# Kernel tuning notes

Hardware: AMD Instinct MI355X
Metric: run time of the kernel (lower is better)

Reference implementation:

```python
import jax, jax.numpy as jnp
import numpy as np

N_NODES = 100000
N_EDGES = 400000
N_GRAPHS = 5000
F_IN = 64
H = 128
OUT = 1
N_LAYERS = 3  # gat_conv + 2 atom_gats
NEG_SLOPE = 0.01


def _gat_conv(x_src, x_dst, src, dst, W, a_src, a_dst, b, num_dst):
    """PyG GATConv, heads=1, add_self_loops=False, negative_slope=0.01.

    x_src: [Ns, Fin], x_dst: [Nd, Fin]; src/dst: [E] int; W: [Fin, H];
    a_src, a_dst, b: [H]. Returns [Nd, H].
    """
    hs = x_src @ W                      # [Ns, H]
    hd = x_dst @ W                      # [Nd, H]
    as_n = hs @ a_src                   # [Ns]
    ad_n = hd @ a_dst                   # [Nd]
    e = jax.nn.leaky_relu(as_n[src] + ad_n[dst], NEG_SLOPE)  # [E]
    # segment softmax over destination nodes
    seg_max = jax.ops.segment_max(e, dst, num_segments=num_dst)
    seg_max = jnp.where(jnp.isfinite(seg_max), seg_max, 0.0)
    ex = jnp.exp(e - seg_max[dst])
    denom = jax.ops.segment_sum(ex, dst, num_segments=num_dst) + 1e-16
    alpha = ex / denom[dst]             # [E]
    out = jax.ops.segment_sum(alpha[:, None] * hs[src], dst, num_segments=num_dst)
    return out + b


def setup_inputs() -> dict:
    key = jax.random.key(0)
    ks = jax.random.split(key, 16)
    x = jax.random.normal(ks[0], (N_NODES, F_IN), dtype=jnp.float32)
    edge_index = jax.random.randint(ks[1], (2, N_EDGES), 0, N_NODES, dtype=jnp.int64)
    batch = jnp.sort(jax.random.randint(ks[2], (N_NODES,), 0, N_GRAPHS, dtype=jnp.int64))
    s_in = 1.0 / np.sqrt(F_IN)
    s_h = 1.0 / np.sqrt(H)
    W1 = jax.random.uniform(ks[3], (F_IN, H), jnp.float32, -s_in, s_in)
    b1 = jax.random.uniform(ks[4], (H,), jnp.float32, -s_in, s_in)
    gW = jax.random.normal(ks[5], (N_LAYERS, H, H), jnp.float32) * s_h
    g_asrc = jax.random.normal(ks[6], (N_LAYERS, H), jnp.float32) * s_h
    g_adst = jax.random.normal(ks[7], (N_LAYERS, H), jnp.float32) * s_h
    g_b = jnp.zeros((N_LAYERS, H), jnp.float32)
    mW = jax.random.normal(ks[8], (H, H), jnp.float32) * s_h
    m_asrc = jax.random.normal(ks[9], (H,), jnp.float32) * s_h
    m_adst = jax.random.normal(ks[10], (H,), jnp.float32) * s_h
    m_b = jnp.zeros((H,), jnp.float32)
    W2 = jax.random.uniform(ks[11], (H, OUT), jnp.float32, -s_h, s_h)
    b2 = jax.random.uniform(ks[12], (OUT,), jnp.float32, -s_h, s_h)
    return {"x": x, "edge_index": edge_index, "batch": batch,
            "W1": W1, "b1": b1, "gW": gW, "g_asrc": g_asrc,
            "g_adst": g_adst, "g_b": g_b, "mW": mW, "m_asrc": m_asrc,
            "m_adst": m_adst, "m_b": m_b, "W2": W2, "b2": b2}


def reference(x, edge_index, batch, W1, b1, gW, g_asrc, g_adst, g_b,
              mW, m_asrc, m_adst, m_b, W2, b2):
    src, dst = edge_index[0], edge_index[1]
    h = jax.nn.leaky_relu(x @ W1 + b1, NEG_SLOPE)            # lin1 + leaky_relu_
    for i in range(N_LAYERS):                                 # gat_conv + atom_gats
        h = jax.nn.elu(_gat_conv(h, h, src, dst, gW[i], g_asrc[i],
                                 g_adst[i], g_b[i], N_NODES))
    # global readout: node -> graph bipartite GAT
    pooled = jax.nn.relu(jax.ops.segment_sum(h, batch, num_segments=N_GRAPHS))
    row = jnp.arange(N_NODES)
    out = jax.nn.elu(_gat_conv(h, pooled, row, batch, mW, m_asrc,
                               m_adst, m_b, N_GRAPHS))
    return out @ W2 + b2                                      # [N_GRAPHS, OUT]
```

## Files before the change

kernel.cpp:

```cpp
#include <hip/hip_runtime.h>
#include <hip/hip_fp16.h>
#include <math.h>
#include <stdint.h>

#define DEV __device__ __forceinline__

using f32x4 = __attribute__((ext_vector_type(4))) float;
using half8 = __attribute__((ext_vector_type(8))) _Float16;
typedef union { uint4 u; half8 h; } u4h8;

DEV float lrelu(float x){ return x > 0.f ? x : 0.01f*x; }
DEV float elu1(float x){ return x > 0.f ? x : __expf(x)-1.f; }

DEV int lower_bound_i(const int* __restrict__ a, int n, int key){
  int lo = 0, hi = n;
  while (lo < hi){ int mid = (lo+hi)>>1; if (a[mid] < key) lo = mid+1; else hi = mid; }
  return lo;
}

__global__ void xprep(const float* __restrict__ x, unsigned short* __restrict__ xh, int n4){
  int i = blockIdx.x*256 + threadIdx.x;
  if (i >= n4) return;
  float4 v = ((const float4*)x)[i];
  __half2 h0 = __floats2half2_rn(v.x, v.y);
  __half2 h1 = __floats2half2_rn(v.z, v.w);
  uint2 o;
  o.x = *(uint32_t*)&h0; o.y = *(uint32_t*)&h1;
  *(uint2*)(xh + (size_t)i*4) = o;
}

__global__ void wprep(const float* __restrict__ W, unsigned short* __restrict__ Hi,
                      unsigned short* __restrict__ Lo, int K, int tot){
  int idx = blockIdx.x*256 + threadIdx.x;
  if (idx >= tot) return;
  int kn = K*128;
  int mat = idx / kn;
  int rem = idx - mat*kn;
  int k = rem >> 7;
  int n = rem & 127;
  float v = W[idx];
  __half h = __float2half_rn(v);
  float lo = (v - __half2float(h)) * 1024.f;
  size_t o = (size_t)mat*kn + (size_t)n*K + k;
  Hi[o] = __half_as_ushort(h);
  Lo[o] = __half_as_ushort(__float2half_rn(lo));
}

template<int KC, int OUTMODE, bool DOTA, bool DOTB>
__global__ __launch_bounds__(256, 3) void gemm_mfma(
    const unsigned short* __restrict__ Ah, const unsigned short* __restrict__ Wt_hi,
    const unsigned short* __restrict__ Wt_lo, const float* __restrict__ bias,
    const float* __restrict__ va, const float* __restrict__ vb,
    unsigned short* __restrict__ Ch,
    float* __restrict__ outa, float* __restrict__ outb, int M)
{
  constexpr int K = KC*32;
  const int tid = threadIdx.x;
  const int lane = tid & 63;
  const int wv = tid >> 6;
  const int ml = lane & 15;
  const int kg = lane >> 4;
  const int R0 = blockIdx.x * 64;

  __shared__ uint32_t sA[2][1024];
  __shared__ float sC[4][32][36];
  __shared__ float sd[4][64][2];

  const unsigned short* bhp[2];
  const unsigned short* blp[2];
  #pragma unroll
  for (int nt = 0; nt < 2; ++nt){
    int n = wv*32 + nt*16 + ml;
    bhp[nt] = Wt_hi + (size_t)n*K + kg*8;
    blp[nt] = Wt_lo + (size_t)n*K + kg*8;
  }

  auto STAGE = [&](int c){
    int o = tid*16;
    int row = o >> 6;
    int t = (o >> 4) & 3;
    int gr = R0 + row; gr = gr < M ? gr : M-1;
    int j = t ^ ((row >> 1) & 3);
    const char* src = (const char*)(Ah + (size_t)gr*K + c*32) + j*16;
    char* dst = (char*)(&sA[c & 1][0]) + wv*1024;
    __builtin_amdgcn_global_load_lds(
        (const __attribute__((address_space(1))) void*)src,
        (__attribute__((address_space(3))) void*)dst, 16, 0, 0);
  };

  f32x4 accH[4][2], accL[4][2];
  #pragma unroll
  for (int mt = 0; mt < 4; ++mt)
    #pragma unroll
    for (int nt = 0; nt < 2; ++nt){
      accH[mt][nt] = (f32x4){0.f,0.f,0.f,0.f};
      accL[mt][nt] = (f32x4){0.f,0.f,0.f,0.f};
    }

  STAGE(0);
  u4h8 bhC[2], blC[2];
  #pragma unroll
  for (int nt = 0; nt < 2; ++nt){
    bhC[nt].u = *(const uint4*)(bhp[nt]);
    blC[nt].u = *(const uint4*)(blp[nt]);
  }
  __syncthreads();

  #pragma unroll
  for (int c = 0; c < KC; ++c){
    u4h8 bhN[2], blN[2];
    if (c + 1 < KC){
      STAGE(c + 1);
      #pragma unroll
      for (int nt = 0; nt < 2; ++nt){
        bhN[nt].u = *(const uint4*)(bhp[nt] + (c+1)*32);
        blN[nt].u = *(const uint4*)(blp[nt] + (c+1)*32);
      }
    }
    const char* buf = (const char*)&sA[c & 1][0];
    #pragma unroll
    for (int mt = 0; mt < 4; ++mt){
      int row = mt*16 + ml;
      int ba = row*64 + ((kg ^ ((row >> 1) & 3)) * 16);
      u4h8 A_;
      A_.u = *(const uint4*)(buf + ba);
      #pragma unroll
      for (int nt = 0; nt < 2; ++nt){
        accH[mt][nt] = __builtin_amdgcn_mfma_f32_16x16x32_f16(A_.h, bhC[nt].h, accH[mt][nt], 0, 0, 0);
        accL[mt][nt] = __builtin_amdgcn_mfma_f32_16x16x32_f16(A_.h, blC[nt].h, accL[mt][nt], 0, 0, 0);
      }
    }
    __syncthreads();
    if (c + 1 < KC){
      #pragma unroll
      for (int nt = 0; nt < 2; ++nt){ bhC[nt] = bhN[nt]; blC[nt] = blN[nt]; }
    }
  }

  #pragma unroll
  for (int mt = 0; mt < 4; ++mt)
    #pragma unroll
    for (int nt = 0; nt < 2; ++nt)
      accH[mt][nt] = accH[mt][nt] + accL[mt][nt] * 9.765625e-4f;

  if constexpr (DOTA || DOTB){
    float vaL[2] = {0.f,0.f}, vbL[2] = {0.f,0.f};
    if constexpr (DOTA){ vaL[0] = va[wv*32 + ml]; vaL[1] = va[wv*32 + 16 + ml]; }
    if constexpr (DOTB){ vbL[0] = vb[wv*32 + ml]; vbL[1] = vb[wv*32 + 16 + ml]; }
    #pragma unroll
    for (int mt = 0; mt < 4; ++mt){
      #pragma unroll
      for (int r = 0; r < 4; ++r){
        float pa = 0.f, pb = 0.f;
        #pragma unroll
        for (int nt = 0; nt < 2; ++nt){
          float v = accH[mt][nt][r];
          if constexpr (DOTA) pa = fmaf(v, vaL[nt], pa);
          if constexpr (DOTB) pb = fmaf(v, vbL[nt], pb);
        }
        #pragma unroll
        for (int o = 8; o; o >>= 1){
          if constexpr (DOTA) pa += __shfl_xor(pa, o, 64);
          if constexpr (DOTB) pb += __shfl_xor(pb, o, 64);
        }
        if (ml == 0){
          int rl = mt*16 + kg*4 + r;
          sd[wv][rl][0] = pa;
          sd[wv][rl][1] = pb;
        }
      }
    }
    __syncthreads();
    if (tid < 64){
      int row = R0 + tid;
      if (row < M){
        if constexpr (DOTA)
          outa[row] = sd[0][tid][0] + sd[1][tid][0] + sd[2][tid][0] + sd[3][tid][0];
        if constexpr (DOTB)
          outb[row] = sd[0][tid][1] + sd[1][tid][1] + sd[2][tid][1] + sd[3][tid][1];
      }
    }
  }

  if constexpr (OUTMODE != 0){
    float bv[2];
    if constexpr (OUTMODE == 1){
      bv[0] = bias[wv*32 + ml];
      bv[1] = bias[wv*32 + 16 + ml];
    }
    #pragma unroll
    for (int p = 0; p < 2; ++p){
      #pragma unroll
      for (int mh = 0; mh < 2; ++mh){
        int mt = p*2 + mh;
        #pragma unroll
        for (int nt = 0; nt < 2; ++nt){
          #pragma unroll
          for (int r = 0; r < 4; ++r){
            float v = accH[mt][nt][r];
            if constexpr (OUTMODE == 1) v = lrelu(v + bv[nt]);
            sC[wv][mh*16 + kg*4 + r][nt*16 + ml] = v;
          }
        }
      }
      #pragma unroll
      for (int j = 0; j < 4; ++j){
        int row_l = j*8 + (lane >> 3);
        int c4 = (lane & 7) * 4;
        int grow = R0 + p*32 + row_l;
        if (grow < M){
          float4 v = *(const float4*)&sC[wv][row_l][c4];
          int gcol = wv*32 + c4;
          __half2 h0 = __floats2half2_rn(v.x, v.y);
          __half2 h1 = __floats2half2_rn(v.z, v.w);
          uint2 o;
          o.x = *(uint32_t*)&h0; o.y = *(uint32_t*)&h1;
          *(uint2*)(Ch + (size_t)grow*128 + gcol) = o;
        }
      }
    }
  }
}

__global__ void hist_k(const int* __restrict__ dstv, int* __restrict__ deg, int E){
  int e = blockIdx.x*256 + threadIdx.x;
  if (e < E) atomicAdd(&deg[dstv[e]], 1);
}

__global__ void scan_sum(const int* __restrict__ deg, int* __restrict__ bsum, int n){
  __shared__ int s4[4];
  int i = blockIdx.x*256 + threadIdx.x;
  int v = (i < n) ? deg[i] : 0;
  #pragma unroll
  for (int o = 32; o; o >>= 1) v += __shfl_down(v, o, 64);
  if ((threadIdx.x & 63) == 0) s4[threadIdx.x >> 6] = v;
  __syncthreads();
  if (threadIdx.x == 0) bsum[blockIdx.x] = s4[0]+s4[1]+s4[2]+s4[3];
}

__global__ void scan_blocksums(int* __restrict__ bsum, int nb){
  __shared__ int s[512];
  int t = threadIdx.x;
  s[t] = (t < nb) ? bsum[t] : 0;
  __syncthreads();
  for (int o = 1; o < 512; o <<= 1){
    int v = s[t];
    int u = (t >= o) ? s[t-o] : 0;
    __syncthreads();
    s[t] = v + u;
    __syncthreads();
  }
  if (t < nb) bsum[t] = t ? s[t-1] : 0;
}

__global__ void scan_final(const int* __restrict__ deg, const int* __restrict__ boff,
    int* __restrict__ rp, int* __restrict__ cur, int n, int E)
{
  __shared__ int wsum[4];
  int i = blockIdx.x*256 + threadIdx.x;
  int lane = threadIdx.x & 63, wv = threadIdx.x >> 6;
  int v = (i < n) ? deg[i] : 0;
  int inc = v;
  #pragma unroll
  for (int o = 1; o < 64; o <<= 1){
    int u = __shfl_up(inc, o, 64);
    if (lane >= o) inc += u;
  }
  if (lane == 63) wsum[wv] = inc;
  __syncthreads();
  int woff = boff[blockIdx.x];
  for (int wq = 0; wq < wv; ++wq) woff += wsum[wq];
  int excl = woff + inc - v;
  if (i < n){ rp[i] = excl; cur[i] = excl; }
  if (blockIdx.x == 0 && threadIdx.x == 0) rp[n] = E;
}

__global__ void scatter_k(const int* __restrict__ srcv, const int* __restrict__ dstv,
                          int* __restrict__ cur, int* __restrict__ ssorted, int E){
  int e = blockIdx.x*256 + threadIdx.x;
  if (e < E){
    int p = atomicAdd(&cur[dstv[e]], 1);
    ssorted[p] = srcv[e];
  }
}

__global__ __launch_bounds__(256) void gat_agg(const int* __restrict__ ssorted,
    const int* __restrict__ rp,
    const float* __restrict__ asn, const float* __restrict__ adn,
    const __half2* __restrict__ hs16, const float* __restrict__ bias,
    __half2* __restrict__ outp, int Nn)
{
  const int lane = threadIdx.x & 63;
  const int wv = threadIdx.x >> 6;
  const int d = blockIdx.x*4 + wv;
  if (d >= Nn) return;
  const int lo = rp[d], hi = rp[d+1];
  const int deg = hi - lo;
  float acc0 = 0.f, acc1 = 0.f;
  if (deg > 0){
    const float ad = adn[d];
    if (deg <= 64){
      int sid = 0; float lg = -1e30f;
      if (lane < deg){
        sid = ssorted[lo + lane];
        lg = lrelu(asn[sid] + ad);
      }
      float m = lg, s;
      if (deg <= 8){
        #pragma unroll
        for (int o = 4; o; o >>= 1) m = fmaxf(m, __shfl_xor(m, o, 64));
        float p = (lane < deg) ? __expf(lg - m) : 0.f;
        s = p;
        #pragma unroll
        for (int o = 4; o; o >>= 1) s += __shfl_xor(s, o, 64);
        float alpha = p * (1.f / (s + 1e-16f));
        float al[8]; __half2 v[8];
        #pragma unroll
        for (int i = 0; i < 8; ++i){
          al[i] = __shfl(alpha, i, 64);
          int sd_ = __shfl(sid, i, 64);
          v[i] = hs16[(size_t)sd_*64 + lane];
        }
        #pragma unroll
        for (int i = 0; i < 8; ++i){
          float2 f = __half22float2(v[i]);
          acc0 = fmaf(al[i], f.x, acc0);
          acc1 = fmaf(al[i], f.y, acc1);
        }
      } else {
        #pragma unroll
        for (int o = 32; o; o >>= 1) m = fmaxf(m, __shfl_xor(m, o, 64));
        float p = (lane < deg) ? __expf(lg - m) : 0.f;
        s = p;
        #pragma unroll
        for (int o = 32; o; o >>= 1) s += __shfl_xor(s, o, 64);
        float alpha = p * (1.f / (s + 1e-16f));
        for (int base = 0; base < deg; base += 8){
          float al[8]; __half2 v[8];
          #pragma unroll
          for (int i = 0; i < 8; ++i){
            int e = base + i;
            al[i] = __shfl(alpha, e, 64);
            int sd_ = __shfl(sid, e, 64);
            v[i] = hs16[(size_t)sd_*64 + lane];
          }
          #pragma unroll
          for (int i = 0; i < 8; ++i){
            float2 f = __half22float2(v[i]);
            acc0 = fmaf(al[i], f.x, acc0);
            acc1 = fmaf(al[i], f.y, acc1);
          }
        }
      }
    } else {
      float m = -1e30f;
      for (int e = lane; e < deg; e += 64){
        int sid = ssorted[lo+e];
        m = fmaxf(m, lrelu(asn[sid] + ad));
      }
      #pragma unroll
      for (int o = 32; o; o >>= 1) m = fmaxf(m, __shfl_xor(m, o, 64));
      float s = 0.f;
      for (int e = lane; e < deg; e += 64){
        int sid = ssorted[lo+e];
        s += __expf(lrelu(asn[sid] + ad) - m);
      }
      #pragma unroll
      for (int o = 32; o; o >>= 1) s += __shfl_xor(s, o, 64);
      float inv = 1.f / (s + 1e-16f);
      for (int e = 0; e < deg; ++e){
        int sid = ssorted[lo+e];
        float a = __expf(lrelu(asn[sid] + ad) - m) * inv;
        float2 f = __half22float2(hs16[(size_t)sid*64 + lane]);
        acc0 = fmaf(a, f.x, acc0);
        acc1 = fmaf(a, f.y, acc1);
      }
    }
  }
  float2 bb = *(const float2*)(bias + lane*2);
  outp[(size_t)d*64 + lane] = __floats2half2_rn(elu1(acc0 + bb.x), elu1(acc1 + bb.y));
}

__global__ __launch_bounds__(128) void pool_relu(const unsigned short* __restrict__ h16,
    const int* __restrict__ batch, unsigned short* __restrict__ pooled, int Nn)
{
  const int g = blockIdx.x;
  const int c = threadIdx.x;
  __shared__ int sb[2];
  if (c < 2) sb[c] = lower_bound_i(batch, Nn, g + c);
  __syncthreads();
  const int lo = sb[0], hi = sb[1];
  float s = 0.f;
  for (int i = lo; i < hi; ++i)
    s += __half2float(__ushort_as_half(h16[(size_t)i*128 + c]));
  pooled[(size_t)g*128 + c] = __half_as_ushort(__float2half_rn(fmaxf(s, 0.f)));
}

__global__ __launch_bounds__(128) void mol_agg(const float* __restrict__ as2,
    const float* __restrict__ ad2, const unsigned short* __restrict__ hs2,
    const int* __restrict__ batch, const float* __restrict__ bias,
    const float* __restrict__ W2, const float* __restrict__ b2,
    float* __restrict__ out, int Nn)
{
  const int g = blockIdx.x;
  const int c = threadIdx.x;
  __shared__ int sb[2];
  __shared__ float red[2];
  if (c < 2) sb[c] = lower_bound_i(batch, Nn, g + c);
  __syncthreads();
  const int lo = sb[0], hi = sb[1];
  const float ad = ad2[g];

  float mt = -1e30f;
  for (int i = lo + c; i < hi; i += 128) mt = fmaxf(mt, lrelu(as2[i] + ad));
  #pragma unroll
  for (int o = 32; o; o >>= 1) mt = fmaxf(mt, __shfl_xor(mt, o, 64));
  if ((c & 63) == 0) red[c >> 6] = mt;
  __syncthreads();
  const float m = fmaxf(red[0], red[1]);

  float st = 0.f;
  for (int i = lo + c; i < hi; i += 128) st += __expf(lrelu(as2[i] + ad) - m);
  #pragma unroll
  for (int o = 32; o; o >>= 1) st += __shfl_xor(st, o, 64);
  __syncthreads();
  if ((c & 63) == 0) red[c >> 6] = st;
  __syncthreads();
  const float inv = 1.f / (red[0] + red[1] + 1e-16f);

  float acc = 0.f;
  for (int i = lo; i < hi; ++i){
    float wgt = __expf(lrelu(as2[i] + ad) - m) * inv;
    acc = fmaf(wgt, __half2float(__ushort_as_half(hs2[(size_t)i*128 + c])), acc);
  }
  float v = elu1(acc + bias[c]);

  float r = v * W2[c];
  #pragma unroll
  for (int o = 32; o; o >>= 1) r += __shfl_xor(r, o, 64);
  __syncthreads();
  if ((c & 63) == 0) red[c >> 6] = r;
  __syncthreads();
  if (c == 0) out[g] = red[0] + red[1] + b2[0];
}

extern "C" void kernel_launch(void* const* d_in, const int* in_sizes, int n_in,
                              void* d_out, int out_size, void* d_ws, size_t ws_size,
                              hipStream_t stream)
{
  const float* x      = (const float*)d_in[0];
  const int*   ei     = (const int*)  d_in[1];
  const int*   batch  = (const int*)  d_in[2];
  const float* W1     = (const float*)d_in[3];
  const float* b1     = (const float*)d_in[4];
  const float* gW     = (const float*)d_in[5];
  const float* g_asrc = (const float*)d_in[6];
  const float* g_adst = (const float*)d_in[7];
  const float* g_b    = (const float*)d_in[8];
  const float* mW     = (const float*)d_in[9];
  const float* m_asrc = (const float*)d_in[10];
  const float* m_adst = (const float*)d_in[11];
  const float* m_b    = (const float*)d_in[12];
  const float* W2     = (const float*)d_in[13];
  const float* b2     = (const float*)d_in[14];

  const int Nn = in_sizes[0] / 64;
  const int E  = in_sizes[1] / 2;
  const int G  = out_size;
  const int NL = in_sizes[5] / (128*128);
  const int* srcv = ei;
  const int* dstv = ei + E;

  char* w = (char*)d_ws;
  unsigned short* h16  = (unsigned short*)w; w += (size_t)Nn*128*2;
  char* R = w; w += (size_t)Nn*128*2;
  unsigned short* xh  = (unsigned short*)R;
  unsigned short* hsR = (unsigned short*)R;
  unsigned short* poolh = (unsigned short*)w; w += (size_t)G*128*2;
  float* asN      = (float*)w; w += (size_t)Nn*4;
  float* adN      = (float*)w; w += (size_t)Nn*4;
  int*   deg      = (int*)w;   w += (size_t)Nn*4;
  int*   rp       = (int*)w;   w += (size_t)(Nn+64)*4;
  int*   cur      = (int*)w;   w += (size_t)Nn*4;
  int*   ssorted  = (int*)w;   w += (size_t)E*4;
  int*   bsum     = (int*)w;   w += 4096;
  unsigned short* w1h = (unsigned short*)w; w += 64*128*2;
  unsigned short* w1l = (unsigned short*)w; w += 64*128*2;
  unsigned short* gwh = (unsigned short*)w; w += (size_t)NL*128*128*2;
  unsigned short* gwl = (unsigned short*)w; w += (size_t)NL*128*128*2;
  unsigned short* mwh = (unsigned short*)w; w += 128*128*2;
  unsigned short* mwl = (unsigned short*)w; w += 128*128*2;

  const int nscan = (Nn + 255)/256;
  const int nrt = (Nn + 63)/64;
  const int grt = (G + 63)/64;

  hipMemsetAsync(deg, 0, (size_t)Nn*4, stream);
  hist_k<<<(E+255)/256, 256, 0, stream>>>(dstv, deg, E);
  scan_sum<<<nscan, 256, 0, stream>>>(deg, bsum, Nn);
  scan_blocksums<<<1, 512, 0, stream>>>(bsum, nscan);
  scan_final<<<nscan, 256, 0, stream>>>(deg, bsum, rp, cur, Nn, E);
  scatter_k<<<(E+255)/256, 256, 0, stream>>>(srcv, dstv, cur, ssorted, E);

  xprep<<<((Nn*64/4)+255)/256, 256, 0, stream>>>(x, xh, Nn*64/4);
  wprep<<<((64*128)+255)/256, 256, 0, stream>>>(W1, w1h, w1l, 64, 64*128);
  wprep<<<((NL*128*128)+255)/256, 256, 0, stream>>>(gW, gwh, gwl, 128, NL*128*128);
  wprep<<<((128*128)+255)/256, 256, 0, stream>>>(mW, mwh, mwl, 128, 128*128);

  gemm_mfma<2, 1, false, false><<<nrt, 256, 0, stream>>>(
      xh, w1h, w1l, b1, nullptr, nullptr, h16, nullptr, nullptr, Nn);

  for (int l = 0; l < NL; ++l){
    gemm_mfma<4, 2, true, true><<<nrt, 256, 0, stream>>>(
        h16, gwh + (size_t)l*128*128, gwl + (size_t)l*128*128, nullptr,
        g_asrc + l*128, g_adst + l*128, hsR, asN, adN, Nn);
    gat_agg<<<(Nn+3)/4, 256, 0, stream>>>(ssorted, rp, asN, adN,
        (const __half2*)hsR, g_b + l*128, (__half2*)h16, Nn);
  }

  pool_relu<<<G, 128, 0, stream>>>(h16, batch, poolh, Nn);
  gemm_mfma<4, 2, true, false><<<nrt, 256, 0, stream>>>(
      h16, mwh, mwl, nullptr, m_asrc, nullptr, hsR, asN, nullptr, Nn);
  gemm_mfma<4, 0, true, false><<<grt, 256, 0, stream>>>(
      poolh, mwh, mwl, nullptr, m_adst, nullptr, nullptr, adN, nullptr, G);
  mol_agg<<<G, 128, 0, stream>>>(asN, adN, hsR, batch, m_b, W2, b2, (float*)d_out, Nn);
}
```

Before: 363.0 us.

## Fuse x conversion into lin1 GEMM, merge readout GEMMs, streamline GAT aggregation

Removes the separate fp32-to-fp16 conversion kernel by converting x directly inside a dedicated lin1 GEMM. The main GEMM now stages two 32-wide K slices per pipeline step, halving the barrier count. The pooled graph features are appended after the node features so a single GEMM computes both the readout source and destination projections. The aggregation kernel uses readlane-based gathers and skips shuffle stages when degree is at most 4. The risks are more LDS use per block and a slightly larger workspace.

```diff
diff --git a/kernel.cpp b/kernel.cpp
--- a/kernel.cpp
+++ b/kernel.cpp
@@ -16,17 +16,6 @@
   int lo = 0, hi = n;
   while (lo < hi){ int mid = (lo+hi)>>1; if (a[mid] < key) lo = mid+1; else hi = mid; }
   return lo;
-}
-
-__global__ void xprep(const float* __restrict__ x, unsigned short* __restrict__ xh, int n4){
-  int i = blockIdx.x*256 + threadIdx.x;
-  if (i >= n4) return;
-  float4 v = ((const float4*)x)[i];
-  __half2 h0 = __floats2half2_rn(v.x, v.y);
-  __half2 h1 = __floats2half2_rn(v.z, v.w);
-  uint2 o;
-  o.x = *(uint32_t*)&h0; o.y = *(uint32_t*)&h1;
-  *(uint2*)(xh + (size_t)i*4) = o;
 }
 
 __global__ void wprep(const float* __restrict__ W, unsigned short* __restrict__ Hi,
@@ -46,15 +35,11 @@
   Lo[o] = __half_as_ushort(__float2half_rn(lo));
 }
 
-template<int KC, int OUTMODE, bool DOTA, bool DOTB>
-__global__ __launch_bounds__(256, 3) void gemm_mfma(
-    const unsigned short* __restrict__ Ah, const unsigned short* __restrict__ Wt_hi,
+__global__ __launch_bounds__(256, 3) void gemm_lin1(
+    const float* __restrict__ X, const unsigned short* __restrict__ Wt_hi,
     const unsigned short* __restrict__ Wt_lo, const float* __restrict__ bias,
-    const float* __restrict__ va, const float* __restrict__ vb,
-    unsigned short* __restrict__ Ch,
-    float* __restrict__ outa, float* __restrict__ outb, int M)
+    unsigned short* __restrict__ Ch, int M)
 {
-  constexpr int K = KC*32;
   const int tid = threadIdx.x;
   const int lane = tid & 63;
   const int wv = tid >> 6;
@@ -64,29 +49,33 @@
 
   __shared__ uint32_t sA[2][1024];
   __shared__ float sC[4][32][36];
-  __shared__ float sd[4][64][2];
 
   const unsigned short* bhp[2];
   const unsigned short* blp[2];
   #pragma unroll
   for (int nt = 0; nt < 2; ++nt){
     int n = wv*32 + nt*16 + ml;
-    bhp[nt] = Wt_hi + (size_t)n*K + kg*8;
-    blp[nt] = Wt_lo + (size_t)n*K + kg*8;
-  }
-
-  auto STAGE = [&](int c){
-    int o = tid*16;
-    int row = o >> 6;
-    int t = (o >> 4) & 3;
+    bhp[nt] = Wt_hi + (size_t)n*64 + kg*8;
+    blp[nt] = Wt_lo + (size_t)n*64 + kg*8;
+  }
+
+  {
+    int row = tid >> 2, kq = tid & 3;
     int gr = R0 + row; gr = gr < M ? gr : M-1;
-    int j = t ^ ((row >> 1) & 3);
-    const char* src = (const char*)(Ah + (size_t)gr*K + c*32) + j*16;
-    char* dst = (char*)(&sA[c & 1][0]) + wv*1024;
-    __builtin_amdgcn_global_load_lds(
-        (const __attribute__((address_space(1))) void*)src,
-        (__attribute__((address_space(3))) void*)dst, 16, 0, 0);
-  };
+    const float4* xp = (const float4*)(X + (size_t)gr*64 + kq*16);
+    int sub = kq >> 1;
+    #pragma unroll
+    for (int i = 0; i < 4; ++i){
+      float4 v = xp[i];
+      __half2 h0 = __floats2half2_rn(v.x, v.y);
+      __half2 h1 = __floats2half2_rn(v.z, v.w);
+      int slot = (kq & 1)*2 + (i >> 1);
+      int slot_s = slot ^ ((row >> 1) & 3);
+      int byte = row*64 + slot_s*16 + (i & 1)*8;
+      *(uint2*)((char*)&sA[sub][0] + byte) = make_uint2(*(uint32_t*)&h0, *(uint32_t*)&h1);
+    }
+  }
+  __syncthreads();
 
   f32x4 accH[4][2], accL[4][2];
   #pragma unroll
@@ -97,27 +86,15 @@
       accL[mt][nt] = (f32x4){0.f,0.f,0.f,0.f};
     }
 
-  STAGE(0);
-  u4h8 bhC[2], blC[2];
-  #pragma unroll
-  for (int nt = 0; nt < 2; ++nt){
-    bhC[nt].u = *(const uint4*)(bhp[nt]);
-    blC[nt].u = *(const uint4*)(blp[nt]);
-  }
-  __syncthreads();
-
-  #pragma unroll
-  for (int c = 0; c < KC; ++c){
-    u4h8 bhN[2], blN[2];
-    if (c + 1 < KC){
-      STAGE(c + 1);
-      #pragma unroll
-      for (int nt = 0; nt < 2; ++nt){
-        bhN[nt].u = *(const uint4*)(bhp[nt] + (c+1)*32);
-        blN[nt].u = *(const uint4*)(blp[nt] + (c+1)*32);
-      }
-    }
-    const char* buf = (const char*)&sA[c & 1][0];
+  #pragma unroll
+  for (int sc = 0; sc < 2; ++sc){
+    u4h8 bh[2], bl[2];
+    #pragma unroll
+    for (int nt = 0; nt < 2; ++nt){
+      bh[nt].u = *(const uint4*)(bhp[nt] + sc*32);
+      bl[nt].u = *(const uint4*)(blp[nt] + sc*32);
+    }
+    const char* buf = (const char*)&sA[sc][0];
     #pragma unroll
     for (int mt = 0; mt < 4; ++mt){
       int row = mt*16 + ml;
@@ -126,14 +103,147 @@
       A_.u = *(const uint4*)(buf + ba);
       #pragma unroll
       for (int nt = 0; nt < 2; ++nt){
-        accH[mt][nt] = __builtin_amdgcn_mfma_f32_16x16x32_f16(A_.h, bhC[nt].h, accH[mt][nt], 0, 0, 0);
-        accL[mt][nt] = __builtin_amdgcn_mfma_f32_16x16x32_f16(A_.h, blC[nt].h, accL[mt][nt], 0, 0, 0);
+        accH[mt][nt] = __builtin_amdgcn_mfma_f32_16x16x32_f16(A_.h, bh[nt].h, accH[mt][nt], 0, 0, 0);
+        accL[mt][nt] = __builtin_amdgcn_mfma_f32_16x16x32_f16(A_.h, bl[nt].h, accL[mt][nt], 0, 0, 0);
+      }
+    }
+  }
+
+  float bv[2] = { bias[wv*32 + ml], bias[wv*32 + 16 + ml] };
+  #pragma unroll
+  for (int p = 0; p < 2; ++p){
+    #pragma unroll
+    for (int mh = 0; mh < 2; ++mh){
+      int mt = p*2 + mh;
+      #pragma unroll
+      for (int nt = 0; nt < 2; ++nt){
+        #pragma unroll
+        for (int r = 0; r < 4; ++r){
+          float v = accH[mt][nt][r] + accL[mt][nt][r] * 9.765625e-4f;
+          v = lrelu(v + bv[nt]);
+          sC[wv][mh*16 + kg*4 + r][nt*16 + ml] = v;
+        }
       }
     }
     __syncthreads();
-    if (c + 1 < KC){
-      #pragma unroll
-      for (int nt = 0; nt < 2; ++nt){ bhC[nt] = bhN[nt]; blC[nt] = blN[nt]; }
+    #pragma unroll
+    for (int j = 0; j < 4; ++j){
+      int row_l = j*8 + (lane >> 3);
+      int c4 = (lane & 7) * 4;
+      int grow = R0 + p*32 + row_l;
+      if (grow < M){
+        float4 v = *(const float4*)&sC[wv][row_l][c4];
+        int gcol = wv*32 + c4;
+        __half2 h0 = __floats2half2_rn(v.x, v.y);
+        __half2 h1 = __floats2half2_rn(v.z, v.w);
+        *(uint2*)(Ch + (size_t)grow*128 + gcol) = make_uint2(*(uint32_t*)&h0, *(uint32_t*)&h1);
+      }
+    }
+    __syncthreads();
+  }
+}
+
+template<int OUTMODE, bool DOTA, bool DOTB>
+__global__ __launch_bounds__(256, 3) void gemm_mfma(
+    const unsigned short* __restrict__ Ah, const unsigned short* __restrict__ Wt_hi,
+    const unsigned short* __restrict__ Wt_lo,
+    const float* __restrict__ va, const float* __restrict__ vb,
+    unsigned short* __restrict__ Ch,
+    float* __restrict__ outa, float* __restrict__ outb, int M)
+{
+  constexpr int K = 128;
+  const int tid = threadIdx.x;
+  const int lane = tid & 63;
+  const int wv = tid >> 6;
+  const int ml = lane & 15;
+  const int kg = lane >> 4;
+  const int R0 = blockIdx.x * 64;
+
+  __shared__ uint32_t sA[4][1024];
+  __shared__ float sC[4][32][36];
+  __shared__ float sd[4][64][2];
+
+  const unsigned short* bhp[2];
+  const unsigned short* blp[2];
+  #pragma unroll
+  for (int nt = 0; nt < 2; ++nt){
+    int n = wv*32 + nt*16 + ml;
+    bhp[nt] = Wt_hi + (size_t)n*K + kg*8;
+    blp[nt] = Wt_lo + (size_t)n*K + kg*8;
+  }
+
+  auto STAGE = [&](int ch){
+    #pragma unroll
+    for (int j = 0; j < 2; ++j){
+      int sc = ch*2 + j;
+      int o = tid*16;
+      int row = o >> 6;
+      int t = (o >> 4) & 3;
+      int gr = R0 + row; gr = gr < M ? gr : M-1;
+      int jj = t ^ ((row >> 1) & 3);
+      const char* src = (const char*)(Ah + (size_t)gr*K + sc*32 + jj*8);
+      char* dst = (char*)(&sA[(ch & 1)*2 + j][0]) + wv*1024;
+      __builtin_amdgcn_global_load_lds(
+          (const __attribute__((address_space(1))) void*)src,
+          (__attribute__((address_space(3))) void*)dst, 16, 0, 0);
+    }
+  };
+
+  f32x4 accH[4][2], accL[4][2];
+  #pragma unroll
+  for (int mt = 0; mt < 4; ++mt)
+    #pragma unroll
+    for (int nt = 0; nt < 2; ++nt){
+      accH[mt][nt] = (f32x4){0.f,0.f,0.f,0.f};
+      accL[mt][nt] = (f32x4){0.f,0.f,0.f,0.f};
+    }
+
+  STAGE(0);
+  u4h8 bh[2][2], bl[2][2];
+  #pragma unroll
+  for (int j = 0; j < 2; ++j)
+    #pragma unroll
+    for (int nt = 0; nt < 2; ++nt){
+      bh[j][nt].u = *(const uint4*)(bhp[nt] + j*32);
+      bl[j][nt].u = *(const uint4*)(blp[nt] + j*32);
+    }
+  __syncthreads();
+
+  #pragma unroll
+  for (int ch = 0; ch < 2; ++ch){
+    u4h8 bhN[2][2], blN[2][2];
+    if (ch == 0){
+      STAGE(1);
+      #pragma unroll
+      for (int j = 0; j < 2; ++j)
+        #pragma unroll
+        for (int nt = 0; nt < 2; ++nt){
+          bhN[j][nt].u = *(const uint4*)(bhp[nt] + (2 + j)*32);
+          blN[j][nt].u = *(const uint4*)(blp[nt] + (2 + j)*32);
+        }
+    }
+    #pragma unroll
+    for (int js = 0; js < 2; ++js){
+      const char* buf = (const char*)&sA[(ch & 1)*2 + js][0];
+      #pragma unroll
+      for (int mt = 0; mt < 4; ++mt){
+        int row = mt*16 + ml;
+        int ba = row*64 + ((kg ^ ((row >> 1) & 3)) * 16);
+        u4h8 A_;
+        A_.u = *(const uint4*)(buf + ba);
+        #pragma unroll
+        for (int nt = 0; nt < 2; ++nt){
+          accH[mt][nt] = __builtin_amdgcn_mfma_f32_16x16x32_f16(A_.h, bh[js][nt].h, accH[mt][nt], 0, 0, 0);
+          accL[mt][nt] = __builtin_amdgcn_mfma_f32_16x16x32_f16(A_.h, bl[js][nt].h, accL[mt][nt], 0, 0, 0);
+        }
+      }
+    }
+    __syncthreads();
+    if (ch == 0){
+      #pragma unroll
+      for (int j = 0; j < 2; ++j)
+        #pragma unroll
+        for (int nt = 0; nt < 2; ++nt){ bh[j][nt] = bhN[j][nt]; bl[j][nt] = blN[j][nt]; }
     }
   }
 
@@ -182,12 +292,8 @@
     }
   }
 
-  if constexpr (OUTMODE != 0){
-    float bv[2];
-    if constexpr (OUTMODE == 1){
-      bv[0] = bias[wv*32 + ml];
-      bv[1] = bias[wv*32 + 16 + ml];
-    }
+  if constexpr (OUTMODE == 2){
+    if constexpr (DOTA || DOTB) __syncthreads();
     #pragma unroll
     for (int p = 0; p < 2; ++p){
       #pragma unroll
@@ -196,13 +302,11 @@
         #pragma unroll
         for (int nt = 0; nt < 2; ++nt){
           #pragma unroll
-          for (int r = 0; r < 4; ++r){
-            float v = accH[mt][nt][r];
-            if constexpr (OUTMODE == 1) v = lrelu(v + bv[nt]);
-            sC[wv][mh*16 + kg*4 + r][nt*16 + ml] = v;
-          }
-        }
-      }
+          for (int r = 0; r < 4; ++r)
+            sC[wv][mh*16 + kg*4 + r][nt*16 + ml] = accH[mt][nt][r];
+        }
+      }
+      __syncthreads();
       #pragma unroll
       for (int j = 0; j < 4; ++j){
         int row_l = j*8 + (lane >> 3);
@@ -213,11 +317,10 @@
           int gcol = wv*32 + c4;
           __half2 h0 = __floats2half2_rn(v.x, v.y);
           __half2 h1 = __floats2half2_rn(v.z, v.w);
-          uint2 o;
-          o.x = *(uint32_t*)&h0; o.y = *(uint32_t*)&h1;
-          *(uint2*)(Ch + (size_t)grow*128 + gcol) = o;
-        }
-      }
+          *(uint2*)(Ch + (size_t)grow*128 + gcol) = make_uint2(*(uint32_t*)&h0, *(uint32_t*)&h1);
+        }
+      }
+      __syncthreads();
     }
   }
 }
@@ -282,6 +385,15 @@
     int p = atomicAdd(&cur[dstv[e]], 1);
     ssorted[p] = srcv[e];
   }
+}
+
+DEV void gstep(const __half2* __restrict__ hs16, int lane, float alpha, int sid, int i,
+               float& a0, float& a1){
+  float al = __uint_as_float(__builtin_amdgcn_readlane(__float_as_uint(alpha), i));
+  int sd = __builtin_amdgcn_readlane(sid, i);
+  float2 f = __half22float2(hs16[(size_t)sd*64 + lane]);
+  a0 = fmaf(al, f.x, a0);
+  a1 = fmaf(al, f.y, a1);
 }
 
 __global__ __launch_bounds__(256) void gat_agg(const int* __restrict__ ssorted,
@@ -305,51 +417,39 @@
         sid = ssorted[lo + lane];
         lg = lrelu(asn[sid] + ad);
       }
-      float m = lg, s;
+      float m = lg;
       if (deg <= 8){
-        #pragma unroll
-        for (int o = 4; o; o >>= 1) m = fmaxf(m, __shfl_xor(m, o, 64));
+        if (deg > 4) m = fmaxf(m, __shfl_xor(m, 4, 64));
+        m = fmaxf(m, __shfl_xor(m, 2, 64));
+        m = fmaxf(m, __shfl_xor(m, 1, 64));
         float p = (lane < deg) ? __expf(lg - m) : 0.f;
-        s = p;
-        #pragma unroll
-        for (int o = 4; o; o >>= 1) s += __shfl_xor(s, o, 64);
+        float s = p;
+        if (deg > 4) s += __shfl_xor(s, 4, 64);
+        s += __shfl_xor(s, 2, 64);
+        s += __shfl_xor(s, 1, 64);
         float alpha = p * (1.f / (s + 1e-16f));
-        float al[8]; __half2 v[8];
-        #pragma unroll
-        for (int i = 0; i < 8; ++i){
-          al[i] = __shfl(alpha, i, 64);
-          int sd_ = __shfl(sid, i, 64);
-          v[i] = hs16[(size_t)sd_*64 + lane];
-        }
-        #pragma unroll
-        for (int i = 0; i < 8; ++i){
-          float2 f = __half22float2(v[i]);
-          acc0 = fmaf(al[i], f.x, acc0);
-          acc1 = fmaf(al[i], f.y, acc1);
+        gstep(hs16, lane, alpha, sid, 0, acc0, acc1);
+        gstep(hs16, lane, alpha, sid, 1, acc0, acc1);
+        gstep(hs16, lane, alpha, sid, 2, acc0, acc1);
+        gstep(hs16, lane, alpha, sid, 3, acc0, acc1);
+        if (deg > 4){
+          gstep(hs16, lane, alpha, sid, 4, acc0, acc1);
+          gstep(hs16, lane, alpha, sid, 5, acc0, acc1);
+          gstep(hs16, lane, alpha, sid, 6, acc0, acc1);
+          gstep(hs16, lane, alpha, sid, 7, acc0, acc1);
         }
       } else {
         #pragma unroll
         for (int o = 32; o; o >>= 1) m = fmaxf(m, __shfl_xor(m, o, 64));
         float p = (lane < deg) ? __expf(lg - m) : 0.f;
-        s = p;
+        float s = p;
         #pragma unroll
         for (int o = 32; o; o >>= 1) s += __shfl_xor(s, o, 64);
         float alpha = p * (1.f / (s + 1e-16f));
         for (int base = 0; base < deg; base += 8){
-          float al[8]; __half2 v[8];
           #pragma unroll
-          for (int i = 0; i < 8; ++i){
-            int e = base + i;
-            al[i] = __shfl(alpha, e, 64);
-            int sd_ = __shfl(sid, e, 64);
-            v[i] = hs16[(size_t)sd_*64 + lane];
-          }
-          #pragma unroll
-          for (int i = 0; i < 8; ++i){
-            float2 f = __half22float2(v[i]);
-            acc0 = fmaf(al[i], f.x, acc0);
-            acc1 = fmaf(al[i], f.y, acc1);
-          }
+          for (int i = 0; i < 8; ++i)
+            gstep(hs16, lane, alpha, sid, base + i, acc0, acc1);
         }
       }
     } else {
@@ -382,7 +482,7 @@
 }
 
 __global__ __launch_bounds__(128) void pool_relu(const unsigned short* __restrict__ h16,
-    const int* __restrict__ batch, unsigned short* __restrict__ pooled, int Nn)
+    const int* __restrict__ batch, unsigned short* __restrict__ ptail, int Nn)
 {
   const int g = blockIdx.x;
   const int c = threadIdx.x;
@@ -393,7 +493,7 @@
   float s = 0.f;
   for (int i = lo; i < hi; ++i)
     s += __half2float(__ushort_as_half(h16[(size_t)i*128 + c]));
-  pooled[(size_t)g*128 + c] = __half_as_ushort(__float2half_rn(fmaxf(s, 0.f)));
+  ptail[(size_t)g*128 + c] = __half_as_ushort(__float2half_rn(fmaxf(s, 0.f)));
 }
 
 __global__ __launch_bounds__(128) void mol_agg(const float* __restrict__ as2,
@@ -468,17 +568,15 @@
   const int E  = in_sizes[1] / 2;
   const int G  = out_size;
   const int NL = in_sizes[5] / (128*128);
+  const int M2 = Nn + G;
   const int* srcv = ei;
   const int* dstv = ei + E;
 
   char* w = (char*)d_ws;
-  unsigned short* h16  = (unsigned short*)w; w += (size_t)Nn*128*2;
-  char* R = w; w += (size_t)Nn*128*2;
-  unsigned short* xh  = (unsigned short*)R;
-  unsigned short* hsR = (unsigned short*)R;
-  unsigned short* poolh = (unsigned short*)w; w += (size_t)G*128*2;
-  float* asN      = (float*)w; w += (size_t)Nn*4;
-  float* adN      = (float*)w; w += (size_t)Nn*4;
+  unsigned short* h16 = (unsigned short*)w; w += (size_t)(M2+64)*128*2;
+  unsigned short* hsR = (unsigned short*)w; w += (size_t)(M2+64)*128*2;
+  float* asO      = (float*)w; w += (size_t)(M2+64)*4;
+  float* adO      = (float*)w; w += (size_t)(M2+64)*4;
   int*   deg      = (int*)w;   w += (size_t)Nn*4;
   int*   rp       = (int*)w;   w += (size_t)(Nn+64)*4;
   int*   cur      = (int*)w;   w += (size_t)Nn*4;
@@ -493,7 +591,7 @@
 
   const int nscan = (Nn + 255)/256;
   const int nrt = (Nn + 63)/64;
-  const int grt = (G + 63)/64;
+  const int mrt = (M2 + 63)/64;
 
   hipMemsetAsync(deg, 0, (size_t)Nn*4, stream);
   hist_k<<<(E+255)/256, 256, 0, stream>>>(dstv, deg, E);
@@ -502,26 +600,22 @@
   scan_final<<<nscan, 256, 0, stream>>>(deg, bsum, rp, cur, Nn, E);
   scatter_k<<<(E+255)/256, 256, 0, stream>>>(srcv, dstv, cur, ssorted, E);
 
-  xprep<<<((Nn*64/4)+255)/256, 256, 0, stream>>>(x, xh, Nn*64/4);
   wprep<<<((64*128)+255)/256, 256, 0, stream>>>(W1, w1h, w1l, 64, 64*128);
   wprep<<<((NL*128*128)+255)/256, 256, 0, stream>>>(gW, gwh, gwl, 128, NL*128*128);
   wprep<<<((128*128)+255)/256, 256, 0, stream>>>(mW, mwh, mwl, 128, 128*128);
 
-  gemm_mfma<2, 1, false, false><<<nrt, 256, 0, stream>>>(
-      xh, w1h, w1l, b1, nullptr, nullptr, h16, nullptr, nullptr, Nn);
+  gemm_lin1<<<nrt, 256, 0, stream>>>(x, w1h, w1l, b1, h16, Nn);
 
   for (int l = 0; l < NL; ++l){
-    gemm_mfma<4, 2, true, true><<<nrt, 256, 0, stream>>>(
-        h16, gwh + (size_t)l*128*128, gwl + (size_t)l*128*128, nullptr,
-        g_asrc + l*128, g_adst + l*128, hsR, asN, adN, Nn);
-    gat_agg<<<(Nn+3)/4, 256, 0, stream>>>(ssorted, rp, asN, adN,
+    gemm_mfma<2, true, true><<<nrt, 256, 0, stream>>>(
+        h16, gwh + (size_t)l*128*128, gwl + (size_t)l*128*128,
+        g_asrc + l*128, g_adst + l*128, hsR, asO, adO, Nn);
+    gat_agg<<<(Nn+3)/4, 256, 0, stream>>>(ssorted, rp, asO, adO,
         (const __half2*)hsR, g_b + l*128, (__half2*)h16, Nn);
   }
 
-  pool_relu<<<G, 128, 0, stream>>>(h16, batch, poolh, Nn);
-  gemm_mfma<4, 2, true, false><<<nrt, 256, 0, stream>>>(
-      h16, mwh, mwl, nullptr, m_asrc, nullptr, hsR, asN, nullptr, Nn);
-  gemm_mfma<4, 0, true, false><<<grt, 256, 0, stream>>>(
-      poolh, mwh, mwl, nullptr, m_adst, nullptr, nullptr, adN, nullptr, G);
-  mol_agg<<<G, 128, 0, stream>>>(asN, adN, hsR, batch, m_b, W2, b2, (float*)d_out, Nn);
-}
+  pool_relu<<<G, 128, 0, stream>>>(h16, batch, h16 + (size_t)Nn*128, Nn);
+  gemm_mfma<2, true, true><<<mrt, 256, 0, stream>>>(
+      h16, mwh, mwl, m_asrc, m_adst, hsR, asO, adO, M2);
+  mol_agg<<<G, 128, 0, stream>>>(asO, adO + Nn, hsR, batch, m_b, W2, b2, (float*)d_out, Nn);
+}
```

Result: faster. 347.7 us (-4.2%).
